# Optimization experiments

Hardware: AMD Instinct MI355X
Metric: run time of the kernel (lower is better)

## Reference

```python
import jax, jax.numpy as jnp
import numpy as np

N = 20000      # nodes
E = 320000     # edges (before self loops)
IN = 128       # in_channels
HID = 64       # hid_channels
H = 4          # in_head
OUT = 16       # out_channels (classes)
SLOPE = 0.2    # GATv2 leaky_relu negative_slope default


def setup_inputs() -> dict:
    key = jax.random.key(0)
    ks = jax.random.split(key, 40)
    d = {}
    d["x"] = jax.random.normal(ks[0], (N, IN), jnp.float32)
    src = jax.random.randint(ks[1], (E,), 0, N)
    dst = jax.random.randint(ks[2], (E,), 0, N)
    d["edge_index"] = jnp.stack([src, dst]).astype(jnp.int32)
    # (in_ch, out_ch_per_head, heads) for the 4 GATv2Conv layers
    dims = [(IN, HID, H), (H * HID, HID, H), (H * HID, HID, H), (H * HID, OUT, 1)]
    ki = 3
    for li, (ic, oc, h) in enumerate(dims, 1):
        sc = 1.0 / np.sqrt(ic)
        d[f"w{li}l"] = jax.random.normal(ks[ki], (h * oc, ic), jnp.float32) * sc; ki += 1
        d[f"b{li}l"] = jnp.zeros((h * oc,), jnp.float32)
        d[f"w{li}r"] = jax.random.normal(ks[ki], (h * oc, ic), jnp.float32) * sc; ki += 1
        d[f"b{li}r"] = jnp.zeros((h * oc,), jnp.float32)
        d[f"a{li}"] = jax.random.normal(ks[ki], (h, oc), jnp.float32) * (1.0 / np.sqrt(oc)); ki += 1
        # output bias: [h*oc] if concat else [oc]; layer 4 is concat=False
        d[f"bo{li}"] = jnp.zeros((h * oc if li < 4 else oc,), jnp.float32)
    return d


def gatv2_layer(x, src, dst, wl, bl, wr, br, att, bias, heads, oc, concat):
    n = x.shape[0]
    xl = (x @ wl.T + bl).reshape(n, heads, oc)   # source transform
    xr = (x @ wr.T + br).reshape(n, heads, oc)   # target transform
    # per-edge GATv2 attention logit: a^T LeakyReLU(x_l[src] + x_r[dst])
    e = jax.nn.leaky_relu(xl[src] + xr[dst], SLOPE)          # [E,H,C]
    logits = jnp.einsum('ehc,hc->eh', e, att)                # [E,H]
    # segment softmax over incoming edges of each dst node
    m = jax.ops.segment_max(logits, dst, num_segments=n)     # [N,H]
    ex = jnp.exp(logits - m[dst])
    den = jax.ops.segment_sum(ex, dst, num_segments=n)
    alpha = ex / den[dst]                                    # [E,H]
    out = jax.ops.segment_sum(alpha[..., None] * xl[src], dst, num_segments=n)  # [N,H,C]
    out = out.reshape(n, heads * oc) if concat else out.mean(axis=1)
    return out + bias


def reference(x, edge_index,
              w1l, b1l, w1r, b1r, a1, bo1,
              w2l, b2l, w2r, b2r, a2, bo2,
              w3l, b3l, w3r, b3r, a3, bo3,
              w4l, b4l, w4r, b4r, a4, bo4):
    n = x.shape[0]
    loop = jnp.arange(n, dtype=edge_index.dtype)
    src = jnp.concatenate([edge_index[0], loop])  # PyG GATv2Conv adds self loops
    dst = jnp.concatenate([edge_index[1], loop])
    h = gatv2_layer(x, src, dst, w1l, b1l, w1r, b1r, a1, bo1, H, HID, True)
    h = jax.nn.relu(h)
    h = gatv2_layer(h, src, dst, w2l, b2l, w2r, b2r, a2, bo2, H, HID, True)
    h = jax.nn.relu(h)
    h = gatv2_layer(h, src, dst, w3l, b3l, w3r, b3r, a3, bo3, H, HID, True)
    h = jax.nn.relu(h)
    h = gatv2_layer(h, src, dst, w4l, b4l, w4r, b4r, a4, bo4, 1, OUT, False)
    return h
```

## Files before the change

kernel.cpp:

```cpp
#include <hip/hip_runtime.h>
#include <hip/hip_bf16.h>
#include <math.h>

#define NNODES 20000
#define NEDGES 320000
#define ETOT   (NEDGES + NNODES)
#define SLOPE  0.2f
#define MAXDEG 96
#define LOG2E  1.44269504088896f

typedef __attribute__((ext_vector_type(8))) short bf16x8;
typedef __attribute__((ext_vector_type(4))) float f32x4;

__device__ inline unsigned short bfbits(float f) {
    __hip_bfloat16 h = __float2bfloat16(f);
    unsigned short u;
    __builtin_memcpy(&u, &h, 2);
    return u;
}
__device__ inline float bf2f(unsigned short u) {
    __hip_bfloat16 h;
    __builtin_memcpy(&h, &u, 2);
    return __bfloat162float(h);
}

__device__ inline void gload_lds16(const unsigned short* g, unsigned short* s) {
    __builtin_amdgcn_global_load_lds(
        (const __attribute__((address_space(1))) unsigned int*)g,
        (__attribute__((address_space(3))) unsigned int*)s, 16, 0, 0);
}

__global__ void slab_fill(const int* __restrict__ ei, int* __restrict__ fill,
                          int* __restrict__ slab) {
    int idx = blockIdx.x * blockDim.x + threadIdx.x;
    if (idx >= ETOT) return;
    int src, dst;
    if (idx < NEDGES) { src = ei[idx]; dst = ei[NEDGES + idx]; }
    else              { src = idx - NEDGES; dst = src; }
    int pos = atomicAdd(&fill[dst], 1);
    if (pos < MAXDEG) slab[dst * MAXDEG + pos] = src;
}

__global__ void bin_hist(const int* __restrict__ fill, int* __restrict__ bcnt) {
    __shared__ int h[32];
    const int t = threadIdx.x;
    if (t < 32) h[t] = 0;
    __syncthreads();
    int n = blockIdx.x * 256 + t;
    if (n < NNODES) atomicAdd(&h[min(fill[n], 31)], 1);
    __syncthreads();
    if (t < 32 && h[t] > 0) atomicAdd(&bcnt[t], h[t]);
}

__global__ void bin_scan(const int* __restrict__ bcnt, int* __restrict__ bfill) {
    if (threadIdx.x == 0) {
        int run = 0;
        for (int i = 0; i < 32; i++) { bfill[i] = run; run += bcnt[i]; }
    }
}

__global__ void bin_place(const int* __restrict__ fill, int* __restrict__ bfill,
                          int* __restrict__ order) {
    __shared__ int h[32];
    __shared__ int base[32];
    const int t = threadIdx.x;
    if (t < 32) h[t] = 0;
    __syncthreads();
    int n = blockIdx.x * 256 + t;
    int bin = 0, loc = 0;
    if (n < NNODES) {
        bin = min(fill[n], 31);
        loc = atomicAdd(&h[bin], 1);
    }
    __syncthreads();
    if (t < 32) base[t] = (h[t] > 0) ? atomicAdd(&bfill[t], h[t]) : 0;
    __syncthreads();
    if (n < NNODES) order[base[bin] + loc] = n;
}

__global__ void convert_x(const float* __restrict__ x, unsigned short* __restrict__ Ap) {
    int idx = blockIdx.x * 256 + threadIdx.x;
    if (idx >= NNODES * 128) return;
    int m = idx >> 7, k = idx & 127;
    float f = x[idx];
    unsigned short hi = bfbits(f);
    unsigned short lo = bfbits(f - bf2f(hi));
    unsigned short* row = Ap + (size_t)m * 256;
    row[k] = hi; row[128 + k] = lo;
}

__global__ void convert_w(const float* __restrict__ w0, const float* __restrict__ w1,
                          unsigned short* __restrict__ Wp, int K, int n0, int ntot) {
    int idx = blockIdx.x * 256 + threadIdx.x;
    if (idx >= ntot * K) return;
    int n = idx / K, k = idx - n * K;
    float f = (n < n0) ? w0[n * K + k] : w1[(n - n0) * K + k];
    unsigned short hi = bfbits(f);
    unsigned short lo = bfbits(f - bf2f(hi));
    unsigned short* row = Wp + (size_t)n * 2 * K;
    row[k] = hi; row[K + k] = lo;
}

template <int NOUT>
__global__ __launch_bounds__(256) void gemm_mfma(
    const unsigned short* __restrict__ Ap, int KK,
    const unsigned short* __restrict__ Wp,
    const float* __restrict__ bias0, const float* __restrict__ bias1,
    float* __restrict__ O0, float* __restrict__ O1)
{
    const int W2K = 2 * KK;

    __shared__ unsigned short AH[2 * 4096];
    __shared__ unsigned short AL[2 * 4096];
    __shared__ unsigned short BH[2 * 4096];
    __shared__ unsigned short BL[2 * 4096];

    int m0, nblk;
    if constexpr (NOUT == 512) {
        const int bid = blockIdx.x;
        const int xcd = bid & 7;
        const int k   = bid >> 3;
        nblk = k & 3;
        const int g = (k >> 2) * 8 + xcd;
        if (g >= (NNODES + 127) / 128) return;
        m0 = g * 128;
    } else {
        nblk = 0;
        m0 = blockIdx.x * 128;
    }
    const int n0 = nblk * 128;

    const int tid = threadIdx.x;
    const int l   = tid & 63;
    const int wid = tid >> 6;
    const int wr  = wid >> 1;
    const int wc  = wid & 1;

    const int srow = l & 15;
    const int skb  = l >> 4;

    int arow0 = m0 + wid * 16 + srow;
    int arow1 = arow0 + 64;
    arow0 = min(arow0, NNODES - 1);
    arow1 = min(arow1, NNODES - 1);
    const unsigned short* ahg0 = Ap + (size_t)arow0 * W2K + skb * 8;
    const unsigned short* ahg1 = Ap + (size_t)arow1 * W2K + skb * 8;
    int nrow0 = min(n0 + wid * 16 + srow, NOUT - 1);
    int nrow1 = min(n0 + wid * 16 + srow + 64, NOUT - 1);
    const unsigned short* bhg0 = Wp + (size_t)nrow0 * W2K + skb * 8;
    const unsigned short* bhg1 = Wp + (size_t)nrow1 * W2K + skb * 8;

    const int f0 = (0 * 4 + wid) * 512;
    const int f1 = (1 * 4 + wid) * 512;

    f32x4 acc[4][4];
    #pragma unroll
    for (int i = 0; i < 4; i++)
        #pragma unroll
        for (int j = 0; j < 4; j++)
            acc[i][j] = (f32x4){0.f, 0.f, 0.f, 0.f};

    const int S = KK >> 5;

    auto STAGE = [&](int buf, int k0) {
        const int bo = buf * 4096;
        gload_lds16(ahg0 + k0,      &AH[bo + f0]);
        gload_lds16(ahg1 + k0,      &AH[bo + f1]);
        gload_lds16(ahg0 + KK + k0, &AL[bo + f0]);
        gload_lds16(ahg1 + KK + k0, &AL[bo + f1]);
        gload_lds16(bhg0 + k0,      &BH[bo + f0]);
        gload_lds16(bhg1 + k0,      &BH[bo + f1]);
        gload_lds16(bhg0 + KK + k0, &BL[bo + f0]);
        gload_lds16(bhg1 + KK + k0, &BL[bo + f1]);
    };

    const int ra = (wr * 4) * 512 + l * 8;
    const int rb = (wc * 4) * 512 + l * 8;

    STAGE(0, 0);
    __syncthreads();

    int cur = 0;
    for (int s = 0; s < S; ++s) {
        if (s + 1 < S) STAGE(cur ^ 1, (s + 1) * 32);

        const int bo = cur * 4096;
        bf16x8 ah[4], al_[4], bh[4], bl[4];
        #pragma unroll
        for (int i = 0; i < 4; i++) {
            ah[i]  = *(const bf16x8*)&AH[bo + ra + i * 512];
            al_[i] = *(const bf16x8*)&AL[bo + ra + i * 512];
            bh[i]  = *(const bf16x8*)&BH[bo + rb + i * 512];
            bl[i]  = *(const bf16x8*)&BL[bo + rb + i * 512];
        }

        #pragma unroll
        for (int mi = 0; mi < 4; mi++)
            #pragma unroll
            for (int ni = 0; ni < 4; ni++) {
                acc[mi][ni] = __builtin_amdgcn_mfma_f32_16x16x32_bf16(ah[mi],  bh[ni], acc[mi][ni], 0, 0, 0);
                acc[mi][ni] = __builtin_amdgcn_mfma_f32_16x16x32_bf16(ah[mi],  bl[ni], acc[mi][ni], 0, 0, 0);
                acc[mi][ni] = __builtin_amdgcn_mfma_f32_16x16x32_bf16(al_[mi], bh[ni], acc[mi][ni], 0, 0, 0);
            }

        __syncthreads();
        cur ^= 1;
    }

    if constexpr (NOUT == 512) {
        #pragma unroll
        for (int mi = 0; mi < 4; mi++) {
            int r0 = m0 + wr * 64 + mi * 16 + (l >> 4) * 4;
            #pragma unroll
            for (int ni = 0; ni < 4; ni++) {
                int c = (nblk & 1) * 128 + wc * 64 + ni * 16 + (l & 15);
                const bool left = (nblk < 2);
                float*       O  = left ? O0 : O1;
                const float* bs = left ? bias0 : bias1;
                const float bv  = bs[c];
                const int head = c >> 6, ch = c & 63;
                #pragma unroll
                for (int r = 0; r < 4; r++) {
                    int m = r0 + r;
                    if (m < NNODES)
                        O[((size_t)head * NNODES + m) * 64 + ch] = acc[mi][ni][r] + bv;
                }
            }
        }
    } else {
        #pragma unroll
        for (int mi = 0; mi < 4; mi++) {
            int r0 = m0 + wr * 64 + mi * 16 + (l >> 4) * 4;
            #pragma unroll
            for (int ni = 0; ni < 4; ni++) {
                int c = wc * 64 + ni * 16 + (l & 15);
                if (c >= 32) continue;
                const float bv = (c < 16) ? bias0[c] : bias1[c - 16];
                #pragma unroll
                for (int r = 0; r < 4; r++) {
                    int m = r0 + r;
                    if (m < NNODES) O0[(size_t)m * 32 + c] = acc[mi][ni][r] + bv;
                }
            }
        }
    }
}

__device__ inline float edge_score(float4 v, float4 xrv, float4 attv) {
    float tx = v.x + xrv.x; tx = fmaxf(tx, SLOPE * tx);
    float ty = v.y + xrv.y; ty = fmaxf(ty, SLOPE * ty);
    float tz = v.z + xrv.z; tz = fmaxf(tz, SLOPE * tz);
    float tw = v.w + xrv.w; tw = fmaxf(tw, SLOPE * tw);
    float s = attv.x * tx + attv.y * ty + attv.z * tz + attv.w * tw;
    s += __shfl_xor(s, 1, 64);
    s += __shfl_xor(s, 2, 64);
    s += __shfl_xor(s, 4, 64);
    s += __shfl_xor(s, 8, 64);
    return s;
}

__global__ __launch_bounds__(256) void gat_attn_head(
    const float* __restrict__ xl, const float* __restrict__ xr,
    const float* __restrict__ att, const float* __restrict__ bo,
    const int* __restrict__ fill, const int* __restrict__ slab,
    const int* __restrict__ order,
    unsigned short* __restrict__ outp)
{
    const int b    = blockIdx.x;
    const int xcd  = b & 7;
    const int head = xcd >> 1;
    const int wid  = threadIdx.x >> 6;
    const int grp  = ((b >> 3) * 2 + (xcd & 1)) * 4 + wid;
    const int lane = threadIdx.x & 63;
    const int sub  = lane >> 4;
    const int c    = lane & 15;

    const int node = order[grp * 4 + sub];
    const unsigned coff = (unsigned)c << 4;

    const char* xlh = (const char*)xl + (size_t)head * (NNODES * 256);
    const char* xrh = (const char*)xr + (size_t)head * (NNODES * 256);

    float4 attv = *(const float4*)&att[head * 64 + c * 4];
    attv.x *= LOG2E; attv.y *= LOG2E; attv.z *= LOG2E; attv.w *= LOG2E;
    const float4 xrv = *(const float4*)(xrh + ((unsigned)node << 8) + coff);
    const float4 bov = *(const float4*)&bo[head * 64 + c * 4];

    const int  deg = min(fill[node], MAXDEG);
    const int* sl  = slab + node * MAXDEG;

    int maxd = deg;
    maxd = max(maxd, __shfl_xor(maxd, 16, 64));
    maxd = max(maxd, __shfl_xor(maxd, 32, 64));

    float  d0 = 0.f, d1 = 0.f, d2 = 0.f, d3 = 0.f;
    float4 a0 = make_float4(0.f, 0.f, 0.f, 0.f);
    float4 a1 = a0, a2 = a0, a3 = a0;

    auto gather = [&](int src) -> float4 {
        return *(const float4*)(xlh + (((unsigned)src << 8) + coff));
    };

    auto batch = [&](float4 v0, float4 v1, float4 v2, float4 v3, int pb) {
        float s0 = edge_score(v0, xrv, attv);
        float s1 = edge_score(v1, xrv, attv);
        float s2 = edge_score(v2, xrv, attv);
        float s3 = edge_score(v3, xrv, attv);
        float p0 = (pb + 0 < deg) ? exp2f(s0) : 0.f;
        float p1 = (pb + 1 < deg) ? exp2f(s1) : 0.f;
        float p2 = (pb + 2 < deg) ? exp2f(s2) : 0.f;
        float p3 = (pb + 3 < deg) ? exp2f(s3) : 0.f;
        d0 += p0; d1 += p1; d2 += p2; d3 += p3;
        a0.x += p0 * v0.x; a0.y += p0 * v0.y; a0.z += p0 * v0.z; a0.w += p0 * v0.w;
        a1.x += p1 * v1.x; a1.y += p1 * v1.y; a1.z += p1 * v1.z; a1.w += p1 * v1.w;
        a2.x += p2 * v2.x; a2.y += p2 * v2.y; a2.z += p2 * v2.z; a2.w += p2 * v2.w;
        a3.x += p3 * v3.x; a3.y += p3 * v3.y; a3.z += p3 * v3.z; a3.w += p3 * v3.w;
    };

    int4 i0 = *(const int4*)sl;
    float4 v0 = gather((0 < deg) ? i0.x : node);
    float4 v1 = gather((1 < deg) ? i0.y : node);
    float4 v2 = gather((2 < deg) ? i0.z : node);
    float4 v3 = gather((3 < deg) ? i0.w : node);
    int4 i1 = *(const int4*)&sl[4];
    float4 w0 = gather((4 < deg) ? i1.x : node);
    float4 w1 = gather((5 < deg) ? i1.y : node);
    float4 w2 = gather((6 < deg) ? i1.z : node);
    float4 w3 = gather((7 < deg) ? i1.w : node);

    int pv = 0, pw = 4;
    for (int p = 8; p < maxd; p += 4) {
        int4 t4 = *(const int4*)&sl[p];
        float4 u0 = gather((p + 0 < deg) ? t4.x : node);
        float4 u1 = gather((p + 1 < deg) ? t4.y : node);
        float4 u2 = gather((p + 2 < deg) ? t4.z : node);
        float4 u3 = gather((p + 3 < deg) ? t4.w : node);
        batch(v0, v1, v2, v3, pv);
        v0 = w0; v1 = w1; v2 = w2; v3 = w3;
        w0 = u0; w1 = u1; w2 = u2; w3 = u3;
        pv = pw; pw = p;
    }
    batch(v0, v1, v2, v3, pv);
    if (maxd > 4) batch(w0, w1, w2, w3, pw);

    const float den = (d0 + d1) + (d2 + d3);
    float4 o;
    o.x = fmaxf(((a0.x + a1.x) + (a2.x + a3.x)) / den + bov.x, 0.f);
    o.y = fmaxf(((a0.y + a1.y) + (a2.y + a3.y)) / den + bov.y, 0.f);
    o.z = fmaxf(((a0.z + a1.z) + (a2.z + a3.z)) / den + bov.z, 0.f);
    o.w = fmaxf(((a0.w + a1.w) + (a2.w + a3.w)) / den + bov.w, 0.f);

    unsigned short* row = outp + (size_t)node * 512 + head * 64 + c * 4;
    ushort4 hv, lv;
    hv.x = bfbits(o.x); hv.y = bfbits(o.y); hv.z = bfbits(o.z); hv.w = bfbits(o.w);
    lv.x = bfbits(o.x - bf2f(hv.x));
    lv.y = bfbits(o.y - bf2f(hv.y));
    lv.z = bfbits(o.z - bf2f(hv.z));
    lv.w = bfbits(o.w - bf2f(hv.w));
    *(ushort4*)(row)       = hv;
    *(ushort4*)(row + 256) = lv;
}

__global__ __launch_bounds__(256) void gat_attn_final(
    const float* __restrict__ O32,
    const float* __restrict__ att, const float* __restrict__ bo,
    const int* __restrict__ fill, const int* __restrict__ slab,
    float* __restrict__ out)
{
    const int lane = threadIdx.x & 63;
    const int sub  = lane >> 4;
    const int c    = lane & 15;

    const int node = (blockIdx.x * 4 + (threadIdx.x >> 6)) * 4 + sub;
    if (node >= NNODES) return;

    const unsigned coff = (unsigned)c << 2;
    const char*    ob   = (const char*)O32;

    const float attc = att[c] * LOG2E;
    const float xrc  = *(const float*)(ob + (((unsigned)node << 7) + 64 + coff));

    const int  deg = min(fill[node], MAXDEG);
    const int* sl  = slab + node * MAXDEG;

    float d0 = 0.f, d1 = 0.f, a0 = 0.f, a1 = 0.f;

    int p = 0;
    for (; p + 2 <= deg; p += 2) {
        int srcA = sl[p];
        int srcB = sl[p + 1];
        float vA = *(const float*)(ob + (((unsigned)srcA << 7) + coff));
        float vB = *(const float*)(ob + (((unsigned)srcB << 7) + coff));
        float tA = vA + xrc; tA = fmaxf(tA, SLOPE * tA);
        float tB = vB + xrc; tB = fmaxf(tB, SLOPE * tB);
        float sA = attc * tA;
        float sB = attc * tB;
        sA += __shfl_xor(sA, 1, 64);  sB += __shfl_xor(sB, 1, 64);
        sA += __shfl_xor(sA, 2, 64);  sB += __shfl_xor(sB, 2, 64);
        sA += __shfl_xor(sA, 4, 64);  sB += __shfl_xor(sB, 4, 64);
        sA += __shfl_xor(sA, 8, 64);  sB += __shfl_xor(sB, 8, 64);
        float pA = exp2f(sA);
        float pB = exp2f(sB);
        d0 += pA; a0 += pA * vA;
        d1 += pB; a1 += pB * vB;
    }
    if (p < deg) {
        int src = sl[p];
        float v = *(const float*)(ob + (((unsigned)src << 7) + coff));
        float t = v + xrc; t = fmaxf(t, SLOPE * t);
        float s = attc * t;
        s += __shfl_xor(s, 1, 64);
        s += __shfl_xor(s, 2, 64);
        s += __shfl_xor(s, 4, 64);
        s += __shfl_xor(s, 8, 64);
        float pw = exp2f(s);
        d0 += pw; a0 += pw * v;
    }

    out[(size_t)node * 16 + c] = (a0 + a1) / (d0 + d1) + bo[c];
}

extern "C" void kernel_launch(void* const* d_in, const int* in_sizes, int n_in,
                              void* d_out, int out_size, void* d_ws, size_t ws_size,
                              hipStream_t stream)
{
    const float* x   = (const float*)d_in[0];
    const int*   ei  = (const int*)d_in[1];
    const float* w1l = (const float*)d_in[2];  const float* b1l = (const float*)d_in[3];
    const float* w1r = (const float*)d_in[4];  const float* b1r = (const float*)d_in[5];
    const float* a1  = (const float*)d_in[6];  const float* bo1 = (const float*)d_in[7];
    const float* w2l = (const float*)d_in[8];  const float* b2l = (const float*)d_in[9];
    const float* w2r = (const float*)d_in[10]; const float* b2r = (const float*)d_in[11];
    const float* a2  = (const float*)d_in[12]; const float* bo2 = (const float*)d_in[13];
    const float* w3l = (const float*)d_in[14]; const float* b3l = (const float*)d_in[15];
    const float* w3r = (const float*)d_in[16]; const float* b3r = (const float*)d_in[17];
    const float* a3  = (const float*)d_in[18]; const float* bo3 = (const float*)d_in[19];
    const float* w4l = (const float*)d_in[20]; const float* b4l = (const float*)d_in[21];
    const float* w4r = (const float*)d_in[22]; const float* b4r = (const float*)d_in[23];
    const float* a4  = (const float*)d_in[24]; const float* bo4 = (const float*)d_in[25];

    char* ws = (char*)d_ws;
    auto carve = [&](size_t bytes) {
        void* p = ws;
        ws += (bytes + 255) & ~(size_t)255;
        return p;
    };
    unsigned short* Ap = (unsigned short*)carve((size_t)NNODES * 512 * sizeof(unsigned short));
    float* xl = (float*)carve((size_t)NNODES * 256 * sizeof(float));
    float* xr = (float*)carve((size_t)NNODES * 256 * sizeof(float));
    float* O32 = xl;
    unsigned short* Wp1 = (unsigned short*)carve((size_t)512 * 256 * sizeof(unsigned short));
    unsigned short* Wp2 = (unsigned short*)carve((size_t)512 * 512 * sizeof(unsigned short));
    unsigned short* Wp3 = (unsigned short*)carve((size_t)512 * 512 * sizeof(unsigned short));
    unsigned short* Wp4 = (unsigned short*)carve((size_t)32 * 512 * sizeof(unsigned short));
    int* fill  = (int*)carve((size_t)NNODES * sizeof(int));
    int* slab  = (int*)carve((size_t)NNODES * MAXDEG * sizeof(int));
    int* bcnt  = (int*)carve(32 * sizeof(int));
    int* bfill = (int*)carve(32 * sizeof(int));
    int* order = (int*)carve((size_t)NNODES * sizeof(int));

    const int eblocks = (ETOT + 255) / 256;
    const int nblocks = (NNODES + 255) / 256;

    convert_x<<<(NNODES * 128 + 255) / 256, 256, 0, stream>>>(x, Ap);
    convert_w<<<(512 * 128 + 255) / 256, 256, 0, stream>>>(w1l, w1r, Wp1, 128, 256, 512);
    convert_w<<<(512 * 256 + 255) / 256, 256, 0, stream>>>(w2l, w2r, Wp2, 256, 256, 512);
    convert_w<<<(512 * 256 + 255) / 256, 256, 0, stream>>>(w3l, w3r, Wp3, 256, 256, 512);
    convert_w<<<(32 * 256 + 255) / 256, 256, 0, stream>>>(w4l, w4r, Wp4, 256, 16, 32);

    hipMemsetAsync(fill, 0, (size_t)NNODES * sizeof(int), stream);
    hipMemsetAsync(bcnt, 0, 32 * sizeof(int), stream);
    slab_fill<<<eblocks, 256, 0, stream>>>(ei, fill, slab);
    bin_hist<<<nblocks, 256, 0, stream>>>(fill, bcnt);
    bin_scan<<<1, 64, 0, stream>>>(bcnt, bfill);
    bin_place<<<nblocks, 256, 0, stream>>>(fill, bfill, order);

    const int g512 = 640;
    const int g32  = (NNODES + 127) / 128;
    const int ah   = 5000;

    gemm_mfma<512><<<g512, 256, 0, stream>>>(Ap, 128, Wp1, b1l, b1r, xl, xr);
    gat_attn_head<<<ah, 256, 0, stream>>>(xl, xr, a1, bo1, fill, slab, order, Ap);

    gemm_mfma<512><<<g512, 256, 0, stream>>>(Ap, 256, Wp2, b2l, b2r, xl, xr);
    gat_attn_head<<<ah, 256, 0, stream>>>(xl, xr, a2, bo2, fill, slab, order, Ap);

    gemm_mfma<512><<<g512, 256, 0, stream>>>(Ap, 256, Wp3, b3l, b3r, xl, xr);
    gat_attn_head<<<ah, 256, 0, stream>>>(xl, xr, a3, bo3, fill, slab, order, Ap);

    gemm_mfma<32><<<g32, 256, 0, stream>>>(Ap, 256, Wp4, b4l, b4r, O32, O32);
    gat_attn_final<<<(NNODES + 15) / 16, 256, 0, stream>>>(O32, a4, bo4, fill, slab, (float*)d_out);
}
```

Baseline: 294.2 us.

## Replace double-buffered K=32 staging with single-buffer K=64 stages in GEMM

The bf16x3 MFMA GEMM drops its two-buffer prefetch pipeline, which staged 32-wide K slices. Each iteration now loads a 64-wide K slice into a single buffer, synchronizes, computes two 32-wide chunks, and synchronizes again. This halves the number of loop iterations and barriers per K. The cost is that global-to-LDS loads no longer overlap with MFMA compute, so each stage has to wait for its loads to finish before computing.

```diff
diff --git a/kernel.cpp b/kernel.cpp
--- a/kernel.cpp
+++ b/kernel.cpp
@@ -110,10 +110,10 @@
 {
     const int W2K = 2 * KK;
 
-    __shared__ unsigned short AH[2 * 4096];
-    __shared__ unsigned short AL[2 * 4096];
-    __shared__ unsigned short BH[2 * 4096];
-    __shared__ unsigned short BL[2 * 4096];
+    __shared__ unsigned short AH[8192];
+    __shared__ unsigned short AL[8192];
+    __shared__ unsigned short BH[8192];
+    __shared__ unsigned short BL[8192];
 
     int m0, nblk;
     if constexpr (NOUT == 512) {
@@ -150,8 +150,8 @@
     const unsigned short* bhg0 = Wp + (size_t)nrow0 * W2K + skb * 8;
     const unsigned short* bhg1 = Wp + (size_t)nrow1 * W2K + skb * 8;
 
-    const int f0 = (0 * 4 + wid) * 512;
-    const int f1 = (1 * 4 + wid) * 512;
+    const int fa0 = (wid * 2) * 512;
+    const int fa1 = ((wid + 4) * 2) * 512;
 
     f32x4 acc[4][4];
     #pragma unroll
@@ -160,51 +160,51 @@
         for (int j = 0; j < 4; j++)
             acc[i][j] = (f32x4){0.f, 0.f, 0.f, 0.f};
 
-    const int S = KK >> 5;
-
-    auto STAGE = [&](int buf, int k0) {
-        const int bo = buf * 4096;
-        gload_lds16(ahg0 + k0,      &AH[bo + f0]);
-        gload_lds16(ahg1 + k0,      &AH[bo + f1]);
-        gload_lds16(ahg0 + KK + k0, &AL[bo + f0]);
-        gload_lds16(ahg1 + KK + k0, &AL[bo + f1]);
-        gload_lds16(bhg0 + k0,      &BH[bo + f0]);
-        gload_lds16(bhg1 + k0,      &BH[bo + f1]);
-        gload_lds16(bhg0 + KK + k0, &BL[bo + f0]);
-        gload_lds16(bhg1 + KK + k0, &BL[bo + f1]);
+    const int S = KK >> 6;
+
+    auto STAGE = [&](int k0) {
+        #pragma unroll
+        for (int c = 0; c < 2; c++) {
+            const int ko = k0 + c * 32;
+            const int dc = c * 512;
+            gload_lds16(ahg0 + ko,      &AH[fa0 + dc]);
+            gload_lds16(ahg1 + ko,      &AH[fa1 + dc]);
+            gload_lds16(ahg0 + KK + ko, &AL[fa0 + dc]);
+            gload_lds16(ahg1 + KK + ko, &AL[fa1 + dc]);
+            gload_lds16(bhg0 + ko,      &BH[fa0 + dc]);
+            gload_lds16(bhg1 + ko,      &BH[fa1 + dc]);
+            gload_lds16(bhg0 + KK + ko, &BL[fa0 + dc]);
+            gload_lds16(bhg1 + KK + ko, &BL[fa1 + dc]);
+        }
     };
 
-    const int ra = (wr * 4) * 512 + l * 8;
-    const int rb = (wc * 4) * 512 + l * 8;
-
-    STAGE(0, 0);
-    __syncthreads();
-
-    int cur = 0;
     for (int s = 0; s < S; ++s) {
-        if (s + 1 < S) STAGE(cur ^ 1, (s + 1) * 32);
-
-        const int bo = cur * 4096;
-        bf16x8 ah[4], al_[4], bh[4], bl[4];
+        STAGE(s * 64);
+        __syncthreads();
+
         #pragma unroll
-        for (int i = 0; i < 4; i++) {
-            ah[i]  = *(const bf16x8*)&AH[bo + ra + i * 512];
-            al_[i] = *(const bf16x8*)&AL[bo + ra + i * 512];
-            bh[i]  = *(const bf16x8*)&BH[bo + rb + i * 512];
-            bl[i]  = *(const bf16x8*)&BL[bo + rb + i * 512];
+        for (int c = 0; c < 2; c++) {
+            bf16x8 ah[4], al_[4], bh[4], bl[4];
+            #pragma unroll
+            for (int i = 0; i < 4; i++) {
+                const int ra = ((wr * 4 + i) * 2 + c) * 512 + l * 8;
+                const int rb = ((wc * 4 + i) * 2 + c) * 512 + l * 8;
+                ah[i]  = *(const bf16x8*)&AH[ra];
+                al_[i] = *(const bf16x8*)&AL[ra];
+                bh[i]  = *(const bf16x8*)&BH[rb];
+                bl[i]  = *(const bf16x8*)&BL[rb];
+            }
+            #pragma unroll
+            for (int mi = 0; mi < 4; mi++)
+                #pragma unroll
+                for (int ni = 0; ni < 4; ni++) {
+                    acc[mi][ni] = __builtin_amdgcn_mfma_f32_16x16x32_bf16(ah[mi],  bh[ni], acc[mi][ni], 0, 0, 0);
+                    acc[mi][ni] = __builtin_amdgcn_mfma_f32_16x16x32_bf16(ah[mi],  bl[ni], acc[mi][ni], 0, 0, 0);
+                    acc[mi][ni] = __builtin_amdgcn_mfma_f32_16x16x32_bf16(al_[mi], bh[ni], acc[mi][ni], 0, 0, 0);
+                }
         }
 
-        #pragma unroll
-        for (int mi = 0; mi < 4; mi++)
-            #pragma unroll
-            for (int ni = 0; ni < 4; ni++) {
-                acc[mi][ni] = __builtin_amdgcn_mfma_f32_16x16x32_bf16(ah[mi],  bh[ni], acc[mi][ni], 0, 0, 0);
-                acc[mi][ni] = __builtin_amdgcn_mfma_f32_16x16x32_bf16(ah[mi],  bl[ni], acc[mi][ni], 0, 0, 0);
-                acc[mi][ni] = __builtin_amdgcn_mfma_f32_16x16x32_bf16(al_[mi], bh[ni], acc[mi][ni], 0, 0, 0);
-            }
-
         __syncthreads();
-        cur ^= 1;
     }
 
     if constexpr (NOUT == 512) {
```

New measurement: 290.7 us. About the same (-1.2%).
